# Kernel optimization log

Hardware: AMD Instinct MI355X
Metric: run time of the kernel (lower is better)

The kernel has to match this reference:

```python
import jax, jax.numpy as jnp
import numpy as np


def _layernorm(x, g, b, eps=1e-5):
    m = x.mean(-1, keepdims=True)
    v = ((x - m) ** 2).mean(-1, keepdims=True)
    return (x - m) * jax.lax.rsqrt(v + eps) * g + b


def _rmsnorm(x, w, eps=1e-6):
    return x * jax.lax.rsqrt((x * x).mean(-1, keepdims=True) + eps) * w


def setup_inputs() -> dict:
    key = jax.random.key(0)
    ks = jax.random.split(key, 8)
    B, T, S, C_img = 1, 3, 880, 3072
    C_mouse, D_hid, Dd = 2, 1024, 64
    vin = C_img + 12 * C_mouse  # 3096 = img_hidden + mouse_dim_in*vae_tcr*windows
    w = lambda k, shp: (jax.random.normal(k, shp, jnp.float32) * 0.02)
    return dict(
        x=jax.random.normal(ks[0], (B, T * S, C_img), jnp.float32),
        condition=jax.random.normal(ks[1], (B, 12, C_mouse), jnp.float32),
        w1=w(ks[2], (vin, D_hid)), b1=jnp.zeros((D_hid,), jnp.float32),
        w2=w(ks[3], (D_hid, D_hid)), b2=jnp.zeros((D_hid,), jnp.float32),
        ln_g=jnp.ones((D_hid,), jnp.float32), ln_b=jnp.zeros((D_hid,), jnp.float32),
        wqkv=w(ks[4], (D_hid, 3 * D_hid)), bqkv=jnp.zeros((3 * D_hid,), jnp.float32),
        qn_w=jnp.ones((Dd,), jnp.float32), kn_w=jnp.ones((Dd,), jnp.float32),
        wproj=w(ks[5], (D_hid, C_img)), bproj=jnp.zeros((C_img,), jnp.float32),
        H=22, W=40, temporal_shape=3, num_frame_per_block=3,
    )


def reference(x, condition, w1, b1, w2, b2, ln_g, ln_b, wqkv, bqkv,
              qn_w, kn_w, wproj, bproj, H, W, temporal_shape, num_frame_per_block):
    B, T_S, C_img = x.shape
    T = temporal_shape
    if condition.shape[1] > 9:
        condition = condition[:, -12:, :]
    _, N_frames, C = condition.shape
    action_len, pad_len = 20, 12
    pad = jnp.zeros((B, action_len - N_frames, C), condition.dtype)
    mouse_padded = jnp.concatenate([pad, condition], axis=1)  # [B, 20, C]
    # windowed gather: fixed small loop over num_frame_per_block (<=3)
    wins = jnp.stack([mouse_padded[:, i * 4:i * 4 + pad_len, :]
                      for i in range(num_frame_per_block)], axis=1)  # [B, F, 12, C]
    gm = wins.reshape(B, num_frame_per_block, pad_len * C)  # [B, F, 12C]
    S = 880  # hardcoded in original forward
    gm = jnp.broadcast_to(gm[:, None], (B, S, num_frame_per_block, pad_len * C))
    gm = gm.reshape(B * S, num_frame_per_block, pad_len * C)
    # fuse broadcast mouse features with image tokens (raw row-major reshape, as in torch)
    fused = jnp.concatenate([x.reshape(B * S, T, C_img), gm], axis=-1)  # [BS, T, C_img+12C]
    h = jax.nn.gelu(fused @ w1 + b1, approximate=True) @ w2 + b2
    h = _layernorm(h, ln_g, ln_b)  # [BS, T, D_hid]
    qkv = h @ wqkv + bqkv  # [BS, T, 3*D_hid]
    Dd = qn_w.shape[0]
    Hh = qkv.shape[-1] // (3 * Dd)
    qkv = qkv.reshape(B * S, T, 3, Hh, Dd)
    q, k, v = qkv[:, :, 0], qkv[:, :, 1], qkv[:, :, 2]
    q = _rmsnorm(q, qn_w).astype(v.dtype)
    k = _rmsnorm(k, kn_w).astype(v.dtype)
    # original flattens to one sequence of BS*T tokens for single_prefill (non-causal)
    N = B * S * T
    qf = q.reshape(N, Hh, Dd)
    kf = k.reshape(N, Hh, Dd)
    vf = v.reshape(N, Hh, Dd)
    scale = 1.0 / np.sqrt(Dd).astype(np.float32)
    scores = jnp.einsum('nhd,mhd->hnm', qf, kf) * scale  # [Hh, N, N]
    attn = jax.nn.softmax(scores, axis=-1)
    o = jnp.einsum('hnm,mhd->nhd', attn, vf)  # [N, Hh, Dd]
    # '(B S) T H D -> B (T S) (H D)'
    o = o.reshape(B, S, T, Hh, Dd).transpose(0, 2, 1, 3, 4).reshape(B, T * S, Hh * Dd)
    out = o @ wproj + bproj
    return x + out
```

## Files before the change

### kernel.cpp

```cpp
#include <hip/hip_runtime.h>
#include <hip/hip_bf16.h>

typedef __attribute__((ext_vector_type(8))) short short8;
typedef __attribute__((ext_vector_type(4))) short short4v;
typedef __attribute__((ext_vector_type(4))) unsigned uint4v;
typedef __attribute__((ext_vector_type(4))) float f32x4;
typedef __attribute__((ext_vector_type(16))) float f32x16;
typedef unsigned short u16;

#define ZERO16 (f32x16){0,0,0,0,0,0,0,0,0,0,0,0,0,0,0,0}

__device__ __forceinline__ float b2f(u16 h) {
    unsigned u = ((unsigned)h) << 16;
    float f; __builtin_memcpy(&f, &u, 4); return f;
}
__device__ __forceinline__ u16 f2b(float f) {
    __hip_bfloat16 h = __float2bfloat16(f);
    u16 r; __builtin_memcpy(&r, &h, 2); return r;
}
__device__ __forceinline__ void gload16(const void* g, void* l) {
    __builtin_amdgcn_global_load_lds(
        (const __attribute__((address_space(1))) unsigned*)g,
        (__attribute__((address_space(3))) unsigned*)l, 16, 0, 0);
}
__device__ __forceinline__ unsigned cvtpk_bf16(float lo, float hi) {
    unsigned d;
    asm("v_cvt_pk_bf16_f32 %0, %1, %2" : "=v"(d) : "v"(lo), "v"(hi));
    return d;
}

#define M_VALID 2640
#define M_PAD   2688
#define K1P     3072
#define DH      1024
#define CIMG    3072
#define NHEAD   16
#define NT      84
#define QG      21
#define NSPLIT  3
#define TILES_PER_SPLIT 28
#define LOG2E   1.4426950408889634f

__global__ __launch_bounds__(256) void build_fused_kernel(
    const float* __restrict__ x, u16* __restrict__ fused)
{
    int n = blockIdx.x;
    int tid = threadIdx.x;
    const float* xr = x + (size_t)n * CIMG;
    u16* fr = fused + (size_t)n * K1P;
    for (int c = tid * 4; c < CIMG; c += 1024) {
        float4 v = *(const float4*)(xr + c);
        short4v w;
        w[0] = (short)f2b(v.x); w[1] = (short)f2b(v.y);
        w[2] = (short)f2b(v.z); w[3] = (short)f2b(v.w);
        *(short4v*)(fr + c) = w;
    }
}

__global__ __launch_bounds__(256) void bias1t_kernel(
    const float* __restrict__ w1, const float* __restrict__ b1,
    const float* __restrict__ cond, float* __restrict__ bias1t)
{
    int t = blockIdx.x;
    int col = blockIdx.y * 256 + threadIdx.x;
    float v = b1[col];
#pragma unroll
    for (int j = 0; j < 24; j++) {
        int f = t * 4 + (j >> 1);
        if (f >= 8) v += cond[(f - 8) * 2 + (j & 1)] * w1[(size_t)(3072 + j) * DH + col];
    }
    bias1t[t * DH + col] = v;
}

__global__ __launch_bounds__(256) void transpose_all_kernel(
    const float* __restrict__ w1, const float* __restrict__ w2,
    const float* __restrict__ wqkv, const float* __restrict__ wproj,
    u16* __restrict__ w1t, u16* __restrict__ w2t,
    u16* __restrict__ wqkvt, u16* __restrict__ wprojt)
{
    int b = blockIdx.x;
    const float* W; u16* Wt; int K, N, ldt, nx;
    if (b < 3072)      {            W = w1;    Wt = w1t;    K = 3072; N = DH;   ldt = 3072; nx = 32; }
    else if (b < 4096) { b -= 3072; W = w2;    Wt = w2t;    K = DH;   N = DH;   ldt = DH;   nx = 32; }
    else if (b < 7168) { b -= 4096; W = wqkv;  Wt = wqkvt;  K = DH;   N = 3072; ldt = DH;   nx = 96; }
    else               { b -= 7168; W = wproj; Wt = wprojt; K = DH;   N = CIMG; ldt = DH;   nx = 96; }
    __shared__ float t[32][33];
    int n0 = (b % nx) * 32, k0 = (b / nx) * 32;
    int x = threadIdx.x & 31, y0 = threadIdx.x >> 5;
    for (int yy = y0; yy < 32; yy += 8) {
        int k = k0 + yy, n = n0 + x;
        t[yy][x] = (k < K && n < N) ? W[(size_t)k * N + n] : 0.f;
    }
    __syncthreads();
    for (int yy = y0; yy < 32; yy += 8) {
        int n = n0 + yy, k = k0 + x;
        if (n < N && k < ldt) Wt[(size_t)n * ldt + k] = f2b(t[x][yy]);
    }
}

template<int EPI, int BM, int BN>
__global__ __launch_bounds__(256) void gemm_kernel(
    const u16* __restrict__ A, const u16* __restrict__ Bt,
    const float* __restrict__ bias, const float* __restrict__ resid,
    u16* __restrict__ Cb, float* __restrict__ Cf,
    int N, int K, int Mvalid)
{
    constexpr int MI  = BM / 32;
    constexpr int NJ  = BN / 32;
    constexpr int CA  = BM / 32;
    constexpr int CB  = BN / 32;
    constexpr unsigned ABYTES = BM * 128;
    constexpr unsigned BBYTES = BN * 128;
    constexpr unsigned STG = 2 * (ABYTES + BBYTES);
    constexpr unsigned CTW = BN + 4;
    constexpr unsigned CTB = BM * CTW * 4;
    constexpr int TPR = 256 / BM;
    __shared__ __align__(16) char smem[STG > CTB ? STG : CTB];

    const int tid = threadIdx.x;
    const int lane = tid & 63, wid = tid >> 6;
    const int l15 = lane & 15, l4 = lane >> 4;

    const int nx = N / BN;
    const int nwg = nx * (M_PAD / BM);
    const int bid = blockIdx.x;
    const int wgid = (bid & 7) * (nwg >> 3) + (bid >> 3);
    const int m0 = (wgid / nx) * BM, n0 = (wgid % nx) * BN;

    const int wr = (wid >> 1) * (BM / 2), wc = (wid & 1) * (BN / 2);

    const int srow = lane >> 3;
    const int scol = ((lane & 7) ^ (lane >> 3)) << 3;

    f32x4 acc[MI][NJ];
#pragma unroll
    for (int i = 0; i < MI; i++)
#pragma unroll
        for (int j = 0; j < NJ; j++) acc[i][j] = (f32x4){0.f, 0.f, 0.f, 0.f};

    const int nt = K >> 6;

    auto stage = [&](int buf, int k0) {
        char* Ab = smem + buf * ABYTES;
        char* Bb = smem + 2 * ABYTES + buf * BBYTES;
#pragma unroll
        for (int i = 0; i < CA; i++) {
            int c = wid * CA + i;
            gload16(A + (size_t)(m0 + c * 8 + srow) * K + k0 + scol,
                    Ab + c * 1024 + lane * 16);
        }
#pragma unroll
        for (int i = 0; i < CB; i++) {
            int c = wid * CB + i;
            gload16(Bt + (size_t)(n0 + c * 8 + srow) * K + k0 + scol,
                    Bb + c * 1024 + lane * 16);
        }
    };

    stage(0, 0);
    __syncthreads();
    int cur = 0;
    for (int t = 0; t < nt; t++) {
        if (t + 1 < nt) stage(cur ^ 1, (t + 1) * 64);
        const char* Ab = smem + cur * ABYTES;
        const char* Bb = smem + 2 * ABYTES + cur * BBYTES;
#pragma unroll
        for (int ki = 0; ki < 2; ki++) {
            short8 af[MI], bfr[NJ];
#pragma unroll
            for (int i = 0; i < MI; i++) {
                int row = wr + i * 16 + l15;
                af[i] = *(const short8*)(Ab + row * 128 + (((ki * 4 + l4) ^ (l15 & 7)) << 4));
            }
#pragma unroll
            for (int j = 0; j < NJ; j++) {
                int row = wc + j * 16 + l15;
                bfr[j] = *(const short8*)(Bb + row * 128 + (((ki * 4 + l4) ^ (l15 & 7)) << 4));
            }
            __builtin_amdgcn_s_setprio(1);
#pragma unroll
            for (int i = 0; i < MI; i++)
#pragma unroll
                for (int j = 0; j < NJ; j++)
                    acc[i][j] = __builtin_amdgcn_mfma_f32_16x16x32_bf16(af[i], bfr[j], acc[i][j], 0, 0, 0);
            __builtin_amdgcn_s_setprio(0);
        }
        __syncthreads();
        cur ^= 1;
    }

    float* Ct = (float*)smem;
#pragma unroll
    for (int i = 0; i < MI; i++)
#pragma unroll
        for (int j = 0; j < NJ; j++)
#pragma unroll
            for (int r = 0; r < 4; r++)
                Ct[(wr + i * 16 + l4 * 4 + r) * CTW + wc + j * 16 + l15] = acc[i][j][r];
    __syncthreads();

    const int row = tid / TPR;
    const int cb  = (tid % TPR) * (BN / TPR);
    const int grow = m0 + row;
    const int gcol = n0 + cb;
    if (EPI == 2) {
        if (grow < Mvalid) {
#pragma unroll
            for (int u = 0; u < BN / (4 * TPR); u++) {
                f32x4 v = *(const f32x4*)&Ct[row * CTW + cb + u * 4];
                float4 bv = *(const float4*)&bias[gcol + u * 4];
                float4 rv = *(const float4*)&resid[(size_t)grow * N + gcol + u * 4];
                float4 o;
                o.x = v[0] + bv.x + rv.x; o.y = v[1] + bv.y + rv.y;
                o.z = v[2] + bv.z + rv.z; o.w = v[3] + bv.w + rv.w;
                *(float4*)&Cf[(size_t)grow * N + gcol + u * 4] = o;
            }
        }
    } else {
        const float* bb = bias + (EPI == 0 ? (size_t)(grow % 3) * N : 0);
        u16 tmp[BN / TPR];
#pragma unroll
        for (int u = 0; u < BN / (4 * TPR); u++) {
            f32x4 v = *(const f32x4*)&Ct[row * CTW + cb + u * 4];
            float4 bv = *(const float4*)&bb[gcol + u * 4];
#pragma unroll
            for (int e = 0; e < 4; e++) {
                float val = v[e] + ((const float*)&bv)[e];
                if (EPI == 0) {
                    float tt = val + 0.044715f * val * val * val;
                    val = 0.5f * val * (1.0f + tanhf(0.7978845608028654f * tt));
                }
                tmp[u * 4 + e] = f2b(val);
            }
        }
#pragma unroll
        for (int u = 0; u < BN / (8 * TPR); u++)
            *(short8*)(Cb + (size_t)grow * N + gcol + u * 8) = *(const short8*)&tmp[u * 8];
    }
}

__global__ __launch_bounds__(256) void ln_kernel(
    const u16* __restrict__ h2, const float* __restrict__ g,
    const float* __restrict__ b, u16* __restrict__ out)
{
    int row = blockIdx.x;
    int tid = threadIdx.x;
    const u16* p = h2 + (size_t)row * DH;
    float v[4];
#pragma unroll
    for (int i = 0; i < 4; i++) v[i] = b2f(p[tid * 4 + i]);
    float s1 = v[0] + v[1] + v[2] + v[3];
    float s2 = v[0]*v[0] + v[1]*v[1] + v[2]*v[2] + v[3]*v[3];
    for (int m = 1; m < 64; m <<= 1) { s1 += __shfl_xor(s1, m); s2 += __shfl_xor(s2, m); }
    __shared__ float a1[4], a2[4];
    int w = tid >> 6;
    if ((tid & 63) == 0) { a1[w] = s1; a2[w] = s2; }
    __syncthreads();
    s1 = a1[0] + a1[1] + a1[2] + a1[3];
    s2 = a2[0] + a2[1] + a2[2] + a2[3];
    float mean = s1 * (1.0f / 1024.0f);
    float var = s2 * (1.0f / 1024.0f) - mean * mean;
    float rs = rsqrtf(var + 1e-5f);
    u16* q = out + (size_t)row * DH;
#pragma unroll
    for (int i = 0; i < 4; i++) {
        int c = tid * 4 + i;
        q[c] = f2b((v[i] - mean) * rs * g[c] + b[c]);
    }
}

__global__ __launch_bounds__(256) void fragmentize_kernel(
    const u16* __restrict__ qkv, const float* __restrict__ qw, const float* __restrict__ kw,
    u16* __restrict__ Qf, u16* __restrict__ Kf, u16* __restrict__ Vf)
{
    __shared__ u16 Vlds[8 * 32 * 80];
    const int kt = blockIdx.x;
    const int hg = blockIdx.y;
    const int tid = threadIdx.x;
    const int t32 = tid >> 3, c8 = tid & 7;
    const int n = kt * 32 + t32;
    const u16* row = qkv + (size_t)n * 3072;

#pragma unroll
    for (int hh = 0; hh < 8; hh++) {
        short8 v = *(const short8*)(row + 2048 + (hg * 8 + hh) * 64 + c8 * 8);
        *(short8*)(&Vlds[(hh * 32 + t32) * 80 + c8 * 8]) = v;
    }

    float sq[8], sk[8];
#pragma unroll
    for (int hh = 0; hh < 8; hh++) {
        int h = hg * 8 + hh;
        short8 qv = *(const short8*)(row + h * 64 + c8 * 8);
        short8 kv = *(const short8*)(row + 1024 + h * 64 + c8 * 8);
        float aq = 0.f, ak = 0.f;
#pragma unroll
        for (int e = 0; e < 8; e++) {
            float fq = b2f((u16)qv[e]); aq += fq * fq;
            float fk = b2f((u16)kv[e]); ak += fk * fk;
        }
        sq[hh] = aq; sk[hh] = ak;
    }
#pragma unroll
    for (int m = 1; m < 8; m <<= 1) {
#pragma unroll
        for (int hh = 0; hh < 8; hh++) {
            sq[hh] += __shfl_xor(sq[hh], m);
            sk[hh] += __shfl_xor(sk[hh], m);
        }
    }

    float qwv[8], kwv[8];
#pragma unroll
    for (int e = 0; e < 8; e++) { qwv[e] = qw[c8 * 8 + e]; kwv[e] = kw[c8 * 8 + e]; }

#pragma unroll
    for (int hh = 0; hh < 8; hh++) {
        int h = hg * 8 + hh;
        float rq = rsqrtf(sq[hh] * (1.0f / 64.0f) + 1e-6f) * (0.125f * LOG2E);
        float rk = rsqrtf(sk[hh] * (1.0f / 64.0f) + 1e-6f);
        short8 qv = *(const short8*)(row + h * 64 + c8 * 8);
        short8 kv = *(const short8*)(row + 1024 + h * 64 + c8 * 8);
        short8 qo, ko;
#pragma unroll
        for (int e = 0; e < 8; e++) {
            qo[e] = (short)f2b(b2f((u16)qv[e]) * rq * qwv[e]);
            ko[e] = (short)f2b(b2f((u16)kv[e]) * rk * kwv[e]);
        }
        size_t base = (((size_t)(h * NT + kt) * 4 + (c8 >> 1)) << 9) + t32 * 16 + (c8 & 1) * 8;
        *(short8*)(Qf + base) = qo;
        *(short8*)(Kf + base) = ko;
    }

    __syncthreads();

    const int fd = tid >> 6;
    const int lkq = (tid & 63) >> 1, lhi = tid & 1;
#pragma unroll
    for (int hh = 0; hh < 8; hh++) {
        int h = hg * 8 + hh;
        short8 o;
#pragma unroll
        for (int e = 0; e < 8; e++)
            o[e] = (short)Vlds[(hh * 32 + (fd & 1) * 16 + lhi * 8 + e) * 80 + (fd >> 1) * 32 + lkq];
        *(short8*)(Vf + (((size_t)(h * NT + kt) * 4 + fd) << 9) + lkq * 16 + lhi * 8) = o;
    }
}

__device__ __forceinline__ void attn_tile(
    f32x16& st, float& lr, f32x16& o0, f32x16& o1, const short8* vv)
{
    float sum = 0.f;
    float p[16];
#pragma unroll
    for (int r = 0; r < 16; r++) { p[r] = __builtin_amdgcn_exp2f(st[r]); sum += p[r]; }
    lr += sum + __shfl_xor(sum, 32);

    unsigned a0 = cvtpk_bf16(p[0], p[1]),   a1 = cvtpk_bf16(p[2], p[3]);
    unsigned a2 = cvtpk_bf16(p[4], p[5]),   a3 = cvtpk_bf16(p[6], p[7]);
    unsigned a4 = cvtpk_bf16(p[8], p[9]),   a5 = cvtpk_bf16(p[10], p[11]);
    unsigned a6 = cvtpk_bf16(p[12], p[13]), a7 = cvtpk_bf16(p[14], p[15]);
    asm("v_permlane32_swap_b32 %0, %1" : "+v"(a0), "+v"(a2));
    asm("v_permlane32_swap_b32 %0, %1" : "+v"(a1), "+v"(a3));
    asm("v_permlane32_swap_b32 %0, %1" : "+v"(a4), "+v"(a6));
    asm("v_permlane32_swap_b32 %0, %1" : "+v"(a5), "+v"(a7));
    uint4v u0 = {a0, a1, a2, a3}, u1 = {a4, a5, a6, a7};
    short8 pa0, pa1;
    __builtin_memcpy(&pa0, &u0, 16);
    __builtin_memcpy(&pa1, &u1, 16);

    __builtin_amdgcn_s_setprio(1);
    o0 = __builtin_amdgcn_mfma_f32_32x32x16_bf16(pa0, vv[0], o0, 0, 0, 0);
    o0 = __builtin_amdgcn_mfma_f32_32x32x16_bf16(pa1, vv[1], o0, 0, 0, 0);
    o1 = __builtin_amdgcn_mfma_f32_32x32x16_bf16(pa0, vv[2], o1, 0, 0, 0);
    o1 = __builtin_amdgcn_mfma_f32_32x32x16_bf16(pa1, vv[3], o1, 0, 0, 0);
    __builtin_amdgcn_s_setprio(0);
}

__global__ __launch_bounds__(256, 4) void attn_kernel(
    const u16* __restrict__ Qf, const u16* __restrict__ Kf,
    const u16* __restrict__ Vf, u16* __restrict__ part, float* __restrict__ ml)
{
    const int nwg = NSPLIT * NHEAD * QG;
    const int bid = blockIdx.x;
    const int wgid = (bid & 7) * (nwg >> 3) + (bid >> 3);
    const int s   = wgid / (NHEAD * QG);
    const int rem = wgid % (NHEAD * QG);
    const int h   = rem / QG;
    const int qg  = rem % QG;
    const int wid = threadIdx.x >> 6;
    const int qt  = qg * 4 + wid;
    const int lane = threadIdx.x & 63;
    const int kq = lane & 31;
    const int hi = lane >> 5;
    const int q0 = qt * 32;
    const int lxy = kq * 16 + hi * 8;
    const u16* Kh = Kf + ((size_t)h * NT * 4 << 9);
    const u16* Vh = Vf + ((size_t)h * NT * 4 << 9);

    short8 qf[4];
#pragma unroll
    for (int d = 0; d < 4; d++)
        qf[d] = *(const short8*)(Qf + (((size_t)(h * NT + qt) * 4 + d) << 9) + lxy);

    f32x16 o0 = ZERO16, o1 = ZERO16;
    float lr = 0.f;

    const int ts0 = s * TILES_PER_SPLIT;
    short8 kf[4];
#pragma unroll
    for (int d = 0; d < 4; d++)
        kf[d] = *(const short8*)(Kh + (((size_t)ts0 * 4 + d) << 9) + lxy);

    for (int i = 0; i < TILES_PER_SPLIT; i++) {
        const int tile = ts0 + i;
        const int k0 = tile * 32;
        short8 vv[4];
#pragma unroll
        for (int fd = 0; fd < 4; fd++)
            vv[fd] = *(const short8*)(Vh + (((size_t)tile * 4 + fd) << 9) + lxy);

        f32x16 st = ZERO16;
        __builtin_amdgcn_s_setprio(1);
#pragma unroll
        for (int d = 0; d < 4; d++)
            st = __builtin_amdgcn_mfma_f32_32x32x16_bf16(kf[d], qf[d], st, 0, 0, 0);
        __builtin_amdgcn_s_setprio(0);

        if (i < TILES_PER_SPLIT - 1) {
#pragma unroll
            for (int d = 0; d < 4; d++)
                kf[d] = *(const short8*)(Kh + (((size_t)(tile + 1) * 4 + d) << 9) + lxy);
        }

        if (k0 + 32 > M_VALID) {
#pragma unroll
            for (int r = 0; r < 16; r++) {
                int key = k0 + (r & 3) + 8 * (r >> 2) + 4 * hi;
                if (key >= M_VALID) st[r] = -3.0e38f;
            }
        }
        attn_tile(st, lr, o0, o1, vv);
    }

#pragma unroll
    for (int r = 0; r < 16; r++) {
        int rl = (r & 3) + 8 * (r >> 2) + 4 * hi;
        int qrow = q0 + rl;
        if (qrow < M_VALID) {
            u16* pp = part + ((size_t)s * M_PAD + qrow) * DH + h * 64;
            pp[kq] = f2b(o0[r]);
            pp[kq + 32] = f2b(o1[r]);
        }
    }
    if (hi == 0 && q0 + kq < M_VALID)
        ml[((size_t)s * NHEAD + h) * M_PAD + q0 + kq] = lr;
}

__global__ __launch_bounds__(256) void attn_merge_kernel(
    const u16* __restrict__ part, const float* __restrict__ ml, u16* __restrict__ obf)
{
    const int q = blockIdx.x;
    const int t = threadIdx.x;
    const int h = t >> 4, i = t & 15;
    float L = 0.f;
#pragma unroll
    for (int s = 0; s < NSPLIT; s++)
        L += ml[((size_t)s * NHEAD + h) * M_PAD + q];
    float inv = 1.0f / L;
    float4 acc = {0.f, 0.f, 0.f, 0.f};
#pragma unroll
    for (int s = 0; s < NSPLIT; s++) {
        short4v v = *(const short4v*)(part + ((size_t)s * M_PAD + q) * DH + h * 64 + i * 4);
        acc.x += b2f((u16)v[0]); acc.y += b2f((u16)v[1]);
        acc.z += b2f((u16)v[2]); acc.w += b2f((u16)v[3]);
    }
    int mrow = (q % 3) * 880 + q / 3;
    short4v w;
    w[0] = (short)f2b(acc.x * inv); w[1] = (short)f2b(acc.y * inv);
    w[2] = (short)f2b(acc.z * inv); w[3] = (short)f2b(acc.w * inv);
    *(short4v*)(obf + (size_t)mrow * DH + h * 64 + i * 4) = w;
}

extern "C" void kernel_launch(void* const* d_in, const int* in_sizes, int n_in,
                              void* d_out, int out_size, void* d_ws, size_t ws_size,
                              hipStream_t stream)
{
    const float* x      = (const float*)d_in[0];
    const float* cond   = (const float*)d_in[1];
    const float* w1     = (const float*)d_in[2];
    const float* b1     = (const float*)d_in[3];
    const float* w2     = (const float*)d_in[4];
    const float* b2     = (const float*)d_in[5];
    const float* ln_g   = (const float*)d_in[6];
    const float* ln_b   = (const float*)d_in[7];
    const float* wqkv   = (const float*)d_in[8];
    const float* bqkv   = (const float*)d_in[9];
    const float* qn_w   = (const float*)d_in[10];
    const float* kn_w   = (const float*)d_in[11];
    const float* wproj  = (const float*)d_in[12];
    const float* bproj  = (const float*)d_in[13];
    float* out = (float*)d_out;

    char* ws = (char*)d_ws;
    size_t off = 0;
    auto alloc = [&](size_t bytes) { size_t o = off; off += (bytes + 255) & ~(size_t)255; return o; };

    size_t off_fused  = alloc((size_t)M_PAD * K1P * 2);
    size_t off_w1t    = alloc((size_t)DH * K1P * 2);
    size_t off_w2t    = alloc((size_t)DH * DH * 2);
    size_t off_wqkvt  = alloc((size_t)3072 * DH * 2);
    size_t off_wprojt = alloc((size_t)CIMG * DH * 2);
    size_t off_h1     = alloc((size_t)M_PAD * DH * 2);
    size_t off_h2     = alloc((size_t)M_PAD * DH * 2);
    size_t off_h2ln   = alloc((size_t)M_PAD * DH * 2);
    size_t off_qkv    = alloc((size_t)M_PAD * 3072 * 2);
    size_t off_qf     = alloc((size_t)NHEAD * NT * 4 * 512 * 2);
    size_t off_kf     = alloc((size_t)NHEAD * NT * 4 * 512 * 2);
    size_t off_vf     = alloc((size_t)NHEAD * NT * 4 * 512 * 2);
    size_t off_obf    = alloc((size_t)M_PAD * DH * 2);
    size_t off_b1t    = alloc((size_t)3 * DH * 4);
    (void)ws_size;

    u16* fused  = (u16*)(ws + off_fused);
    u16* w1t    = (u16*)(ws + off_w1t);
    u16* w2t    = (u16*)(ws + off_w2t);
    u16* wqkvt  = (u16*)(ws + off_wqkvt);
    u16* wprojt = (u16*)(ws + off_wprojt);
    u16* h1     = (u16*)(ws + off_h1);
    u16* h2     = (u16*)(ws + off_h2);
    u16* h2ln   = (u16*)(ws + off_h2ln);
    u16* qkvb   = (u16*)(ws + off_qkv);
    u16* Qf     = (u16*)(ws + off_qf);
    u16* Kf     = (u16*)(ws + off_kf);
    u16* Vf     = (u16*)(ws + off_vf);
    u16* obf    = (u16*)(ws + off_obf);
    float* b1t  = (float*)(ws + off_b1t);
    u16* part   = (u16*)(ws + off_h1);
    float* mlbf = (float*)(ws + off_fused);

    build_fused_kernel<<<M_VALID, 256, 0, stream>>>(x, fused);
    bias1t_kernel<<<dim3(3, 4), 256, 0, stream>>>(w1, b1, cond, b1t);
    transpose_all_kernel<<<10240, 256, 0, stream>>>(w1, w2, wqkv, wproj, w1t, w2t, wqkvt, wprojt);

    gemm_kernel<0, 64, 64><<<dim3((DH / 64) * (M_PAD / 64)), 256, 0, stream>>>(fused, w1t, b1t, nullptr, h1, nullptr, DH, K1P, M_PAD);
    gemm_kernel<1, 64, 64><<<dim3((DH / 64) * (M_PAD / 64)), 256, 0, stream>>>(h1, w2t, b2, nullptr, h2, nullptr, DH, DH, M_PAD);
    ln_kernel<<<M_PAD, 256, 0, stream>>>(h2, ln_g, ln_b, h2ln);
    gemm_kernel<1, 128, 128><<<dim3((3072 / 128) * (M_PAD / 128)), 256, 0, stream>>>(h2ln, wqkvt, bqkv, nullptr, qkvb, nullptr, 3072, DH, M_PAD);
    fragmentize_kernel<<<dim3(NT, 2), 256, 0, stream>>>(qkvb, qn_w, kn_w, Qf, Kf, Vf);
    attn_kernel<<<dim3(NSPLIT * NHEAD * QG), 256, 0, stream>>>(Qf, Kf, Vf, part, mlbf);
    attn_merge_kernel<<<M_VALID, 256, 0, stream>>>(part, mlbf, obf);
    gemm_kernel<2, 128, 128><<<dim3((CIMG / 128) * (M_PAD / 128)), 256, 0, stream>>>(obf, wprojt, bproj, x, nullptr, out, CIMG, DH, M_VALID);
}
```

Before: 188.3 us.

## Split-K the first MLP GEMM into three slices with a separate reduce+GELU kernel

The first GEMM now runs with 128x128 tiles and three K-splits of 1024 each, selected by block index. Each split writes fp32 partial sums to a workspace buffer. A new reduce_gelu kernel adds the three partials and the per-frame bias, applies tanh-GELU and writes bf16 h1. The aim is better operand reuse and enough blocks to fill the GPU, at the cost of extra fp32 partial traffic and one more kernel launch.

```diff
diff --git a/kernel.cpp b/kernel.cpp
--- a/kernel.cpp
+++ b/kernel.cpp
@@ -103,7 +103,7 @@
     const u16* __restrict__ A, const u16* __restrict__ Bt,
     const float* __restrict__ bias, const float* __restrict__ resid,
     u16* __restrict__ Cb, float* __restrict__ Cf,
-    int N, int K, int Mvalid)
+    int N, int K, int lda, int ldb, int Mvalid)
 {
     constexpr int MI  = BM / 32;
     constexpr int NJ  = BN / 32;
@@ -121,9 +121,16 @@
     const int lane = tid & 63, wid = tid >> 6;
     const int l15 = lane & 15, l4 = lane >> 4;
 
+    int bid = blockIdx.x;
+    if (EPI == 3) {
+        int sk = bid % 3;
+        bid /= 3;
+        A  += (size_t)sk * K;
+        Bt += (size_t)sk * K;
+        Cf += (size_t)sk * M_PAD * (size_t)N;
+    }
     const int nx = N / BN;
     const int nwg = nx * (M_PAD / BM);
-    const int bid = blockIdx.x;
     const int wgid = (bid & 7) * (nwg >> 3) + (bid >> 3);
     const int m0 = (wgid / nx) * BM, n0 = (wgid % nx) * BN;
 
@@ -146,13 +153,13 @@
 #pragma unroll
         for (int i = 0; i < CA; i++) {
             int c = wid * CA + i;
-            gload16(A + (size_t)(m0 + c * 8 + srow) * K + k0 + scol,
+            gload16(A + (size_t)(m0 + c * 8 + srow) * lda + k0 + scol,
                     Ab + c * 1024 + lane * 16);
         }
 #pragma unroll
         for (int i = 0; i < CB; i++) {
             int c = wid * CB + i;
-            gload16(Bt + (size_t)(n0 + c * 8 + srow) * K + k0 + scol,
+            gload16(Bt + (size_t)(n0 + c * 8 + srow) * ldb + k0 + scol,
                     Bb + c * 1024 + lane * 16);
         }
     };
@@ -203,7 +210,14 @@
     const int cb  = (tid % TPR) * (BN / TPR);
     const int grow = m0 + row;
     const int gcol = n0 + cb;
-    if (EPI == 2) {
+    if (EPI == 3) {
+#pragma unroll
+        for (int u = 0; u < BN / (4 * TPR); u++) {
+            f32x4 v = *(const f32x4*)&Ct[row * CTW + cb + u * 4];
+            float4 o; o.x = v[0]; o.y = v[1]; o.z = v[2]; o.w = v[3];
+            *(float4*)&Cf[(size_t)grow * N + gcol + u * 4] = o;
+        }
+    } else if (EPI == 2) {
         if (grow < Mvalid) {
 #pragma unroll
             for (int u = 0; u < BN / (4 * TPR); u++) {
@@ -217,26 +231,41 @@
             }
         }
     } else {
-        const float* bb = bias + (EPI == 0 ? (size_t)(grow % 3) * N : 0);
         u16 tmp[BN / TPR];
 #pragma unroll
         for (int u = 0; u < BN / (4 * TPR); u++) {
             f32x4 v = *(const f32x4*)&Ct[row * CTW + cb + u * 4];
-            float4 bv = *(const float4*)&bb[gcol + u * 4];
-#pragma unroll
-            for (int e = 0; e < 4; e++) {
-                float val = v[e] + ((const float*)&bv)[e];
-                if (EPI == 0) {
-                    float tt = val + 0.044715f * val * val * val;
-                    val = 0.5f * val * (1.0f + tanhf(0.7978845608028654f * tt));
-                }
-                tmp[u * 4 + e] = f2b(val);
-            }
+            float4 bv = *(const float4*)&bias[gcol + u * 4];
+#pragma unroll
+            for (int e = 0; e < 4; e++)
+                tmp[u * 4 + e] = f2b(v[e] + ((const float*)&bv)[e]);
         }
 #pragma unroll
         for (int u = 0; u < BN / (8 * TPR); u++)
             *(short8*)(Cb + (size_t)grow * N + gcol + u * 8) = *(const short8*)&tmp[u * 8];
     }
+}
+
+__global__ __launch_bounds__(256) void reduce_gelu_kernel(
+    const float* __restrict__ part, const float* __restrict__ bias1t,
+    u16* __restrict__ h1)
+{
+    const int row = blockIdx.x;
+    const int col = threadIdx.x * 4;
+    const size_t base = (size_t)row * DH + col;
+    f32x4 a = *(const f32x4*)&part[base];
+    f32x4 b = *(const f32x4*)&part[(size_t)M_PAD * DH + base];
+    f32x4 c = *(const f32x4*)&part[(size_t)2 * M_PAD * DH + base];
+    float4 bv = *(const float4*)&bias1t[(row % 3) * DH + col];
+    short4v w;
+#pragma unroll
+    for (int e = 0; e < 4; e++) {
+        float val = a[e] + b[e] + c[e] + ((const float*)&bv)[e];
+        float tt = val + 0.044715f * val * val * val;
+        val = 0.5f * val * (1.0f + tanhf(0.7978845608028654f * tt));
+        w[e] = (short)f2b(val);
+    }
+    *(short4v*)(h1 + base) = w;
 }
 
 __global__ __launch_bounds__(256) void ln_kernel(
@@ -536,19 +565,25 @@
     u16* Vf     = (u16*)(ws + off_vf);
     u16* obf    = (u16*)(ws + off_obf);
     float* b1t  = (float*)(ws + off_b1t);
-    u16* part   = (u16*)(ws + off_h1);
+    float* gpart = (float*)(ws + off_h2);
+    u16* apart  = (u16*)(ws + off_h1);
     float* mlbf = (float*)(ws + off_fused);
 
     build_fused_kernel<<<M_VALID, 256, 0, stream>>>(x, fused);
     bias1t_kernel<<<dim3(3, 4), 256, 0, stream>>>(w1, b1, cond, b1t);
     transpose_all_kernel<<<10240, 256, 0, stream>>>(w1, w2, wqkv, wproj, w1t, w2t, wqkvt, wprojt);
 
-    gemm_kernel<0, 64, 64><<<dim3((DH / 64) * (M_PAD / 64)), 256, 0, stream>>>(fused, w1t, b1t, nullptr, h1, nullptr, DH, K1P, M_PAD);
-    gemm_kernel<1, 64, 64><<<dim3((DH / 64) * (M_PAD / 64)), 256, 0, stream>>>(h1, w2t, b2, nullptr, h2, nullptr, DH, DH, M_PAD);
+    gemm_kernel<3, 128, 128><<<dim3(3 * (DH / 128) * (M_PAD / 128)), 256, 0, stream>>>(
+        fused, w1t, nullptr, nullptr, nullptr, gpart, DH, 1024, K1P, K1P, M_PAD);
+    reduce_gelu_kernel<<<M_PAD, 256, 0, stream>>>(gpart, b1t, h1);
+    gemm_kernel<1, 64, 64><<<dim3((DH / 64) * (M_PAD / 64)), 256, 0, stream>>>(
+        h1, w2t, b2, nullptr, h2, nullptr, DH, DH, DH, DH, M_PAD);
     ln_kernel<<<M_PAD, 256, 0, stream>>>(h2, ln_g, ln_b, h2ln);
-    gemm_kernel<1, 128, 128><<<dim3((3072 / 128) * (M_PAD / 128)), 256, 0, stream>>>(h2ln, wqkvt, bqkv, nullptr, qkvb, nullptr, 3072, DH, M_PAD);
+    gemm_kernel<1, 128, 128><<<dim3((3072 / 128) * (M_PAD / 128)), 256, 0, stream>>>(
+        h2ln, wqkvt, bqkv, nullptr, qkvb, nullptr, 3072, DH, DH, DH, M_PAD);
     fragmentize_kernel<<<dim3(NT, 2), 256, 0, stream>>>(qkvb, qn_w, kn_w, Qf, Kf, Vf);
-    attn_kernel<<<dim3(NSPLIT * NHEAD * QG), 256, 0, stream>>>(Qf, Kf, Vf, part, mlbf);
-    attn_merge_kernel<<<M_VALID, 256, 0, stream>>>(part, mlbf, obf);
-    gemm_kernel<2, 128, 128><<<dim3((CIMG / 128) * (M_PAD / 128)), 256, 0, stream>>>(obf, wprojt, bproj, x, nullptr, out, CIMG, DH, M_VALID);
-}
+    attn_kernel<<<dim3(NSPLIT * NHEAD * QG), 256, 0, stream>>>(Qf, Kf, Vf, apart, mlbf);
+    attn_merge_kernel<<<M_VALID, 256, 0, stream>>>(apart, mlbf, obf);
+    gemm_kernel<2, 128, 128><<<dim3((CIMG / 128) * (M_PAD / 128)), 256, 0, stream>>>(
+        obf, wprojt, bproj, x, nullptr, out, CIMG, DH, DH, DH, M_VALID);
+}
```

Measured after the change: 194.5 us. 1.03x slower.
